# Kernel optimization log

Hardware: AMD Instinct MI355X
Metric: run time of the kernel (lower is better)

Reference implementation:

```python
import jax, jax.numpy as jnp
import numpy as np

EPS = 1e-6
DIM = 384; HEADS = 6; POINTS = 4; LEVELS = 3; HIDDEN = 96
B = 2; H0 = 48; W0 = 48

def layernorm(x, w, b):
    m = jnp.mean(x, -1, keepdims=True)
    v = jnp.var(x, -1, keepdims=True)
    return (x - m) * jax.lax.rsqrt(v + EPS) * w + b

def make_ref_points(shapes):
    # normalized (x, y) pixel centers concatenated over levels -> [N, 2]
    pts = []
    for (Hl, Wl) in shapes:
        ry = (jnp.arange(Hl, dtype=jnp.float32) + 0.5) / Hl
        rx = (jnp.arange(Wl, dtype=jnp.float32) + 0.5) / Wl
        gy, gx = jnp.meshgrid(ry, rx, indexing='ij')
        pts.append(jnp.stack([gx.ravel(), gy.ravel()], -1))
    return jnp.concatenate(pts, 0)

def bilinear_gather(v, x, y, Hl, Wl):
    # v: [B, heads, Hl*Wl, c]; x, y: [B, heads, M] pixel coords
    # matches torch grid_sample(bilinear, align_corners=False, padding zeros)
    x0f = jnp.floor(x); y0f = jnp.floor(y)
    wx = (x - x0f)[..., None]; wy = (y - y0f)[..., None]
    x0 = x0f.astype(jnp.int32); y0 = y0f.astype(jnp.int32)
    def tap(yy, xx):
        valid = ((yy >= 0) & (yy < Hl) & (xx >= 0) & (xx < Wl)).astype(v.dtype)
        idx = jnp.clip(yy, 0, Hl - 1) * Wl + jnp.clip(xx, 0, Wl - 1)
        return jnp.take_along_axis(v, idx[..., None], axis=2) * valid[..., None]
    return (tap(y0, x0) * (1 - wx) * (1 - wy) + tap(y0, x0 + 1) * wx * (1 - wy)
            + tap(y0 + 1, x0) * (1 - wx) * wy + tap(y0 + 1, x0 + 1) * wx * wy)

def msdeform_attn(q, f, shapes, Wv, bv, Woff, boff, Watt, batt, Wout, bout):
    Bq, Nq, C = q.shape
    c = C // HEADS
    value = (f @ Wv + bv).reshape(Bq, -1, HEADS, c)
    off = (q @ Woff + boff).reshape(Bq, Nq, HEADS, LEVELS, POINTS, 2)
    att = jax.nn.softmax((q @ Watt + batt).reshape(Bq, Nq, HEADS, LEVELS * POINTS), -1)
    att = att.reshape(Bq, Nq, HEADS, LEVELS, POINTS)
    ref = make_ref_points(shapes)  # [Nq, 2]
    norm = jnp.array([[wl, hl] for (hl, wl) in shapes], dtype=q.dtype)  # [L, 2] = (W, H)
    loc = ref[None, :, None, None, None, :] + off / norm[None, None, None, :, None, :]
    starts = np.cumsum([0] + [h * w for (h, w) in shapes])
    out = jnp.zeros((Bq, Nq, HEADS, c), q.dtype)
    for l, (Hl, Wl) in enumerate(shapes):
        vl = value[:, starts[l]:starts[l + 1]].transpose(0, 2, 1, 3)  # [B,h,HW,c]
        ll = loc[:, :, :, l]  # [B,N,h,P,2]
        x = (ll[..., 0] * Wl - 0.5).transpose(0, 2, 1, 3).reshape(Bq, HEADS, Nq * POINTS)
        y = (ll[..., 1] * Hl - 0.5).transpose(0, 2, 1, 3).reshape(Bq, HEADS, Nq * POINTS)
        s = bilinear_gather(vl, x, y, Hl, Wl).reshape(Bq, HEADS, Nq, POINTS, c)
        out = out + jnp.einsum('bhnpc,bnhp->bnhc', s, att[:, :, :, l])
    return out.reshape(Bq, Nq, C) @ Wout + bout

def dwconv_levels(x, shapes, dw_w, dw_b):
    Bq, N, C = x.shape
    outs, s = [], 0
    for (Hl, Wl) in shapes:
        xi = x[:, s:s + Hl * Wl].reshape(Bq, Hl, Wl, C)
        yi = jax.lax.conv_general_dilated(xi, dw_w, (1, 1), 'SAME',
             dimension_numbers=('NHWC', 'HWIO', 'NHWC'), feature_group_count=C) + dw_b
        outs.append(yi.reshape(Bq, Hl * Wl, C))
        s += Hl * Wl
    return jnp.concatenate(outs, 1)

def setup_inputs():
    key = jax.random.key(0)
    ks = jax.random.split(key, 16)
    n = (H0 * W0) // 4
    N = 21 * n
    wfn = lambda k, s: 0.02 * jax.random.normal(k, s, jnp.float32)
    ones = lambda s: jnp.ones(s, jnp.float32)
    zeros = lambda s: jnp.zeros(s, jnp.float32)
    return {
        'query': jax.random.normal(ks[0], (B, N, DIM), jnp.float32),
        'reference_points': jax.random.uniform(ks[1], (B, N, 1, 2), dtype=jnp.float32),
        'feat': jax.random.normal(ks[2], (B, 4 * n, DIM), jnp.float32),
        'spatial_shapes': jnp.array([[2 * H0, 2 * W0], [H0, W0], [H0 // 2, W0 // 2]], jnp.int32),
        'level_start_index': jnp.array([0, 16 * n, 20 * n], jnp.int32),
        'H': H0, 'W': W0,
        'cti_qnorm_w': ones((DIM,)), 'cti_qnorm_b': zeros((DIM,)),
        'cti_fnorm_w': ones((DIM,)), 'cti_fnorm_b': zeros((DIM,)),
        'cf_qnorm_w': ones((DIM,)), 'cf_qnorm_b': zeros((DIM,)),
        'cf_fnorm_w': ones((DIM,)), 'cf_fnorm_b': zeros((DIM,)),
        'Wv': wfn(ks[3], (DIM, DIM)), 'bv': zeros((DIM,)),
        'Woff': wfn(ks[4], (DIM, HEADS * LEVELS * POINTS * 2)), 'boff': zeros((HEADS * LEVELS * POINTS * 2,)),
        'Watt': wfn(ks[5], (DIM, HEADS * LEVELS * POINTS)), 'batt': zeros((HEADS * LEVELS * POINTS,)),
        'Wout': wfn(ks[6], (DIM, DIM)), 'bout': zeros((DIM,)),
        'ffn_norm_w': ones((DIM,)), 'ffn_norm_b': zeros((DIM,)),
        'fc1_w': wfn(ks[7], (DIM, HIDDEN)), 'fc1_b': zeros((HIDDEN,)),
        'dw_w': wfn(ks[8], (3, 3, 1, HIDDEN)), 'dw_b': zeros((HIDDEN,)),
        'fc2_w': wfn(ks[9], (HIDDEN, DIM)), 'fc2_b': zeros((DIM,)),
    }

def reference(query, reference_points, feat, spatial_shapes, level_start_index, H, W,
              cti_qnorm_w, cti_qnorm_b, cti_fnorm_w, cti_fnorm_b,
              cf_qnorm_w, cf_qnorm_b, cf_fnorm_w, cf_fnorm_b,
              Wv, bv, Woff, boff, Watt, batt, Wout, bout,
              ffn_norm_w, ffn_norm_b, fc1_w, fc1_b, dw_w, dw_b, fc2_w, fc2_b):
    # NOTE: passed reference_points/spatial_shapes/level_start_index are ignored by
    # CTI_toC.forward; it recomputes them via deform_inputs_only_one(query, 16H, 16W).
    Bq, N, C = query.shape
    n = N // 21
    q = jnp.concatenate([query[:, :16 * n], query[:, 16 * n:20 * n] + feat, query[:, 20 * n:]], 1)
    shapes = [(2 * H, 2 * W), (H, W), (H // 2, W // 2)]
    qn = layernorm(q, cti_qnorm_w, cti_qnorm_b)
    fn = layernorm(q, cti_fnorm_w, cti_fnorm_b)
    aq = layernorm(qn, cf_qnorm_w, cf_qnorm_b)
    af = layernorm(fn, cf_fnorm_w, cf_fnorm_b)
    attn = msdeform_attn(aq, af, shapes, Wv, bv, Woff, boff, Watt, batt, Wout, bout)
    out = qn + attn
    h = layernorm(out, ffn_norm_w, ffn_norm_b) @ fc1_w + fc1_b
    h = dwconv_levels(h, shapes, dw_w, dw_b)
    h = jax.nn.gelu(h, approximate=False)
    h = h @ fc2_w + fc2_b
    return out + h
```

## Files before the change

kernel.cpp:

```cpp
#include <hip/hip_runtime.h>
#include <hip/hip_bf16.h>
#include <hip/hip_fp16.h>
#include <cstdint>
#include <cstddef>

#define NB 2
#define NTOK 12096
#define TOKS (NB * NTOK)
#define DIMC 384
#define NHEADS 6
#define CHD 64

typedef __attribute__((ext_vector_type(8))) __bf16 bf16x8;
typedef __attribute__((ext_vector_type(4))) float f32x4;

__device__ __forceinline__ float wave_reduce_add(float v) {
#pragma unroll
  for (int o = 32; o > 0; o >>= 1) v += __shfl_xor(v, o, 64);
  return v;
}

__device__ __forceinline__ float bf_lo(uint u) {
  union { uint i; float f; } c; c.i = u << 16; return c.f;
}
__device__ __forceinline__ float bf_hi(uint u) {
  union { uint i; float f; } c; c.i = u & 0xffff0000u; return c.f;
}
__device__ __forceinline__ ushort f2bf(float x) {
  union { __hip_bfloat16 b; ushort u; } c; c.b = __float2bfloat16(x); return c.u;
}

__device__ __forceinline__ int xcd_chunk(int bid, int nwg) {
  int xcd = bid & 7, off = bid >> 3;
  int q = nwg >> 3, r = nwg & 7;
  return (xcd < r ? xcd * (q + 1) : r * (q + 1) + (xcd - r) * q) + off;
}

__device__ __forceinline__ void gload16(const ushort* g, ushort* l) {
  __builtin_amdgcn_global_load_lds(
      (const __attribute__((address_space(1))) uint*)g,
      (__attribute__((address_space(3))) uint*)l, 16, 0, 0);
}

__global__ __launch_bounds__(256) void prelude_kernel(
    const float* __restrict__ Wv, const float* __restrict__ Woff,
    const float* __restrict__ Watt, const float* __restrict__ Wo,
    const float* __restrict__ fc1, const float* __restrict__ fc2,
    const float* __restrict__ boff, const float* __restrict__ batt,
    const float* __restrict__ fc1b,
    __hip_bfloat16* __restrict__ Wvt, __hip_bfloat16* __restrict__ Wot,
    __hip_bfloat16* __restrict__ Wofat, __hip_bfloat16* __restrict__ fc1t,
    __hip_bfloat16* __restrict__ fc2t, float* __restrict__ bofat,
    float* __restrict__ fc1bp,
    const float* __restrict__ query, const float* __restrict__ feat,
    const float* __restrict__ w1, const float* __restrict__ b1,
    const float* __restrict__ w2, const float* __restrict__ b2,
    const float* __restrict__ w3, const float* __restrict__ b3,
    const float* __restrict__ w4, const float* __restrict__ b4,
    __hip_bfloat16* __restrict__ qn, __hip_bfloat16* __restrict__ aq,
    __hip_bfloat16* __restrict__ af) {
  if (blockIdx.x < 576) {
    int id = blockIdx.x * 256 + threadIdx.x;
    int k = id % 384, n = id / 384;
    Wvt[(size_t)n * 384 + k] = __float2bfloat16(Wv[(size_t)k * 384 + n]);
    Wot[(size_t)n * 384 + k] = __float2bfloat16(Wo[(size_t)k * 384 + n]);
    if (n < 256) {
      float v = 0.f;
      if (n < 144) v = Woff[(size_t)k * 144 + n];
      else if (n < 216) v = Watt[(size_t)k * 72 + (n - 144)];
      Wofat[(size_t)n * 384 + k] = __float2bfloat16(v);
    }
    if (n < 128)
      fc1t[(size_t)n * 384 + k] = __float2bfloat16(n < 96 ? fc1[(size_t)k * 96 + n] : 0.f);
    if (k < 96)
      fc2t[(size_t)n * 96 + k] = __float2bfloat16(fc2[(size_t)k * 384 + n]);
    if (id < 256) bofat[id] = id < 144 ? boff[id] : (id < 216 ? batt[id - 144] : 0.f);
    if (id < 128) fc1bp[id] = id < 96 ? fc1b[id] : 0.f;
    return;
  }

  int wid = ((blockIdx.x - 576) * blockDim.x + threadIdx.x) >> 6;
  if (wid >= TOKS) return;
  int lane = threadIdx.x & 63;
  int bb = wid / NTOK;
  int nq = wid - bb * NTOK;

  float x[6];
  const float* qp = query + (size_t)wid * DIMC + lane;
#pragma unroll
  for (int i = 0; i < 6; ++i) x[i] = qp[64 * i];
  if (nq >= 9216 && nq < 11520) {
    const float* fp = feat + ((size_t)bb * 2304 + (nq - 9216)) * DIMC + lane;
#pragma unroll
    for (int i = 0; i < 6; ++i) x[i] += fp[64 * i];
  }

  float s = 0.f, ss = 0.f;
#pragma unroll
  for (int i = 0; i < 6; ++i) { s += x[i]; ss += x[i] * x[i]; }
  s = wave_reduce_add(s); ss = wave_reduce_add(ss);
  float mean = s * (1.f / DIMC);
  float rs = rsqrtf(ss * (1.f / DIMC) - mean * mean + 1e-6f);

  float qv[6], fv[6];
  __hip_bfloat16* qnp = qn + (size_t)wid * DIMC + lane;
#pragma unroll
  for (int i = 0; i < 6; ++i) {
    int e = lane + 64 * i;
    float xh = (x[i] - mean) * rs;
    qv[i] = xh * w1[e] + b1[e];
    fv[i] = xh * w2[e] + b2[e];
    qnp[64 * i] = __float2bfloat16(qv[i]);
  }

  s = 0.f; ss = 0.f;
#pragma unroll
  for (int i = 0; i < 6; ++i) { s += qv[i]; ss += qv[i] * qv[i]; }
  s = wave_reduce_add(s); ss = wave_reduce_add(ss);
  float m2 = s * (1.f / DIMC);
  float rs2 = rsqrtf(ss * (1.f / DIMC) - m2 * m2 + 1e-6f);
  __hip_bfloat16* aqp = aq + (size_t)wid * DIMC + lane;
#pragma unroll
  for (int i = 0; i < 6; ++i) {
    int e = lane + 64 * i;
    aqp[64 * i] = __float2bfloat16((qv[i] - m2) * rs2 * w3[e] + b3[e]);
  }

  s = 0.f; ss = 0.f;
#pragma unroll
  for (int i = 0; i < 6; ++i) { s += fv[i]; ss += fv[i] * fv[i]; }
  s = wave_reduce_add(s); ss = wave_reduce_add(ss);
  float m3 = s * (1.f / DIMC);
  float rs3 = rsqrtf(ss * (1.f / DIMC) - m3 * m3 + 1e-6f);
  __hip_bfloat16* afp = af + (size_t)wid * DIMC + lane;
#pragma unroll
  for (int i = 0; i < 6; ++i) {
    int e = lane + 64 * i;
    afp[64 * i] = __float2bfloat16((fv[i] - m3) * rs3 * w4[e] + b4[e]);
  }
}

__global__ __launch_bounds__(256) void ln_kernel(
    const float* __restrict__ x, const float* __restrict__ w,
    const float* __restrict__ b, __hip_bfloat16* __restrict__ y) {
  int wid = (blockIdx.x * blockDim.x + threadIdx.x) >> 6;
  if (wid >= TOKS) return;
  int lane = threadIdx.x & 63;
  float v[6];
  const float* xp = x + (size_t)wid * DIMC + lane;
#pragma unroll
  for (int i = 0; i < 6; ++i) v[i] = xp[64 * i];
  float s = 0.f, ss = 0.f;
#pragma unroll
  for (int i = 0; i < 6; ++i) { s += v[i]; ss += v[i] * v[i]; }
  s = wave_reduce_add(s); ss = wave_reduce_add(ss);
  float mean = s * (1.f / DIMC);
  float rs = rsqrtf(ss * (1.f / DIMC) - mean * mean + 1e-6f);
  __hip_bfloat16* yp = y + (size_t)wid * DIMC + lane;
#pragma unroll
  for (int i = 0; i < 6; ++i) {
    int e = lane + 64 * i;
    yp[64 * i] = __float2bfloat16((v[i] - mean) * rs * w[e] + b[e]);
  }
}

template <int EPI, int OUTBF16>
__global__ __launch_bounds__(256) void gemm_mfma(
    const __hip_bfloat16* __restrict__ A, const __hip_bfloat16* __restrict__ Wt,
    const float* __restrict__ bias, const void* __restrict__ Rv,
    void* __restrict__ Cv, int K, int Np, int ntx) {
  __shared__ __align__(16) ushort As[2 * 128 * 32];
  __shared__ __align__(16) ushort Bs[2 * 128 * 32];
  const int tid = threadIdx.x;
  const int tile = xcd_chunk(blockIdx.x, gridDim.x);
  const int tx = tile % ntx, ty = tile / ntx;
  const int m0 = ty * 128, n0 = tx * 128;

  const int lane = tid & 63, wv = tid >> 6;
  const int wm = (wv >> 1) * 64, wn = (wv & 1) * 64;
  const int rl = lane & 15, kb = lane >> 4;

  const int c0 = wv * 64 + lane;
  const int c1 = c0 + 256;
  const int r0c = c0 >> 2, b0 = (c0 & 3) ^ (r0c & 3);
  const int r1c = c1 >> 2, b1 = (c1 & 3) ^ (r1c & 3);
  const ushort* gA0 = (const ushort*)A + (size_t)(m0 + r0c) * K + b0 * 8;
  const ushort* gA1 = (const ushort*)A + (size_t)(m0 + r1c) * K + b1 * 8;
  const ushort* gB0 = (const ushort*)Wt + (size_t)(n0 + r0c) * K + b0 * 8;
  const ushort* gB1 = (const ushort*)Wt + (size_t)(n0 + r1c) * K + b1 * 8;
  ushort* lA0 = &As[(size_t)wv * 512];
  ushort* lA1 = &As[(size_t)wv * 512 + 2048];
  ushort* lB0 = &Bs[(size_t)wv * 512];
  ushort* lB1 = &Bs[(size_t)wv * 512 + 2048];

  f32x4 acc[4][4] = {};
  const int nt = K >> 5;

  gload16(gA0, lA0);
  gload16(gA1, lA1);
  gload16(gB0, lB0);
  gload16(gB1, lB1);
  __syncthreads();

  for (int t = 0; t < nt; ++t) {
    const int cb = (t & 1) << 12;
    const int nb = 4096 - cb;
    if (t + 1 < nt) {
      const int k1 = (t + 1) << 5;
      gload16(gA0 + k1, lA0 + nb);
      gload16(gA1 + k1, lA1 + nb);
      gload16(gB0 + k1, lB0 + nb);
      gload16(gB1 + k1, lB1 + nb);
    }
    bf16x8 avf[4], bvf[4];
#pragma unroll
    for (int i = 0; i < 4; ++i) {
      int ra = wm + i * 16 + rl;
      avf[i] = *(const bf16x8*)&As[cb + ra * 32 + ((kb ^ (ra & 3)) << 3)];
      int rb = wn + i * 16 + rl;
      bvf[i] = *(const bf16x8*)&Bs[cb + rb * 32 + ((kb ^ (rb & 3)) << 3)];
    }
#pragma unroll
    for (int i = 0; i < 4; ++i)
#pragma unroll
      for (int j = 0; j < 4; ++j)
        acc[i][j] = __builtin_amdgcn_mfma_f32_16x16x32_bf16(avf[i], bvf[j],
                                                            acc[i][j], 0, 0, 0);
    __syncthreads();
  }

#pragma unroll
  for (int i = 0; i < 4; ++i) {
#pragma unroll
    for (int j = 0; j < 4; ++j) {
      int col = n0 + wn + j * 16 + rl;
      float bsv = bias[col];
#pragma unroll
      for (int rr = 0; rr < 4; ++rr) {
        int row = m0 + wm + i * 16 + kb * 4 + rr;
        size_t o = (size_t)row * Np + col;
        float v = acc[i][j][rr] + bsv;
        if (EPI == 1) v += __bfloat162float(((const __hip_bfloat16*)Rv)[o]);
        if (EPI == 2) v += ((const float*)Cv)[o];
        if (OUTBF16) ((__hip_bfloat16*)Cv)[o] = __float2bfloat16(v);
        else ((float*)Cv)[o] = v;
      }
    }
  }
}

__global__ __launch_bounds__(256) void gemm_dual(
    const __hip_bfloat16* __restrict__ A1, const __hip_bfloat16* __restrict__ W1,
    const float* __restrict__ bias1, void* __restrict__ C1,
    const __hip_bfloat16* __restrict__ A2, const __hip_bfloat16* __restrict__ W2,
    const float* __restrict__ bias2, void* __restrict__ C2) {
  __shared__ __align__(16) ushort As[2 * 128 * 32];
  __shared__ __align__(16) ushort Bs[2 * 128 * 32];
  const int tid = threadIdx.x;
  const int gbid = blockIdx.x;
  const bool r2 = gbid >= 567;
  const __hip_bfloat16* A = r2 ? A2 : A1;
  const __hip_bfloat16* Wt = r2 ? W2 : W1;
  const float* bias = r2 ? bias2 : bias1;
  void* Cv = r2 ? C2 : C1;
  const int Np = r2 ? 256 : 384, ntx = r2 ? 2 : 3;
  const int lbid = r2 ? gbid - 567 : gbid;
  const int lnwg = r2 ? 378 : 567;
  const int K = 384;

  const int tile = xcd_chunk(lbid, lnwg);
  const int tx = tile % ntx, ty = tile / ntx;
  const int m0 = ty * 128, n0 = tx * 128;

  const int lane = tid & 63, wv = tid >> 6;
  const int wm = (wv >> 1) * 64, wn = (wv & 1) * 64;
  const int rl = lane & 15, kb = lane >> 4;

  const int c0 = wv * 64 + lane;
  const int c1 = c0 + 256;
  const int r0c = c0 >> 2, b0 = (c0 & 3) ^ (r0c & 3);
  const int r1c = c1 >> 2, b1 = (c1 & 3) ^ (r1c & 3);
  const ushort* gA0 = (const ushort*)A + (size_t)(m0 + r0c) * K + b0 * 8;
  const ushort* gA1 = (const ushort*)A + (size_t)(m0 + r1c) * K + b1 * 8;
  const ushort* gB0 = (const ushort*)Wt + (size_t)(n0 + r0c) * K + b0 * 8;
  const ushort* gB1 = (const ushort*)Wt + (size_t)(n0 + r1c) * K + b1 * 8;
  ushort* lA0 = &As[(size_t)wv * 512];
  ushort* lA1 = &As[(size_t)wv * 512 + 2048];
  ushort* lB0 = &Bs[(size_t)wv * 512];
  ushort* lB1 = &Bs[(size_t)wv * 512 + 2048];

  f32x4 acc[4][4] = {};
  const int nt = K >> 5;

  gload16(gA0, lA0);
  gload16(gA1, lA1);
  gload16(gB0, lB0);
  gload16(gB1, lB1);
  __syncthreads();

  for (int t = 0; t < nt; ++t) {
    const int cb = (t & 1) << 12;
    const int nb = 4096 - cb;
    if (t + 1 < nt) {
      const int k1 = (t + 1) << 5;
      gload16(gA0 + k1, lA0 + nb);
      gload16(gA1 + k1, lA1 + nb);
      gload16(gB0 + k1, lB0 + nb);
      gload16(gB1 + k1, lB1 + nb);
    }
    bf16x8 avf[4], bvf[4];
#pragma unroll
    for (int i = 0; i < 4; ++i) {
      int ra = wm + i * 16 + rl;
      avf[i] = *(const bf16x8*)&As[cb + ra * 32 + ((kb ^ (ra & 3)) << 3)];
      int rb = wn + i * 16 + rl;
      bvf[i] = *(const bf16x8*)&Bs[cb + rb * 32 + ((kb ^ (rb & 3)) << 3)];
    }
#pragma unroll
    for (int i = 0; i < 4; ++i)
#pragma unroll
      for (int j = 0; j < 4; ++j)
        acc[i][j] = __builtin_amdgcn_mfma_f32_16x16x32_bf16(avf[i], bvf[j],
                                                            acc[i][j], 0, 0, 0);
    __syncthreads();
  }

#pragma unroll
  for (int i = 0; i < 4; ++i) {
#pragma unroll
    for (int j = 0; j < 4; ++j) {
      int col = n0 + wn + j * 16 + rl;
      float bsv = bias[col];
#pragma unroll
      for (int rr = 0; rr < 4; ++rr) {
        int row = m0 + wm + i * 16 + kb * 4 + rr;
        size_t o = (size_t)row * Np + col;
        float v = acc[i][j][rr] + bsv;
        if (!r2) ((__hip_bfloat16*)Cv)[o] = __float2bfloat16(v);
        else ((float*)Cv)[o] = v;
      }
    }
  }
}

__global__ __launch_bounds__(256) void msdeform_prep(
    const float* __restrict__ offatt, uint* __restrict__ taps) {
  int tile = xcd_chunk(blockIdx.x, gridDim.x);
  int id = tile * 256 + (int)threadIdx.x;
  if (id >= TOKS * 72) return;
  int t = id / 72, r = id - t * 72;
  int h = r / 12, lp = r - h * 12;
  int l = lp >> 2;
  int nq = t % NTOK;

  int pos, Hq, Wq;
  if (nq < 9216)       { pos = nq;         Hq = 96; Wq = 96; }
  else if (nq < 11520) { pos = nq - 9216;  Hq = 48; Wq = 48; }
  else                 { pos = nq - 11520; Hq = 24; Wq = 24; }
  int iq = pos / Wq, jq = pos - iq * Wq;
  float refx = (jq + 0.5f) / (float)Wq;
  float refy = (iq + 0.5f) / (float)Hq;

  const float* lg = offatt + (size_t)t * 256 + 144 + h * 12;
  float mx = -1e30f;
#pragma unroll
  for (int i = 0; i < 12; ++i) mx = fmaxf(mx, lg[i]);
  float sden = 0.f;
#pragma unroll
  for (int i = 0; i < 12; ++i) sden += __expf(lg[i] - mx);
  float aw = __expf(lg[lp] - mx) / sden;

  float ox = offatt[(size_t)t * 256 + h * 24 + lp * 2 + 0];
  float oy = offatt[(size_t)t * 256 + h * 24 + lp * 2 + 1];

  int Wl = 96 >> l;

  float xx = refx * (float)Wl + ox - 0.5f;
  float yy = refy * (float)Wl + oy - 0.5f;
  float x0f = floorf(xx), y0f = floorf(yy);
  int x0 = (int)x0f, y0 = (int)y0f;
  float wx = xx - x0f, wy = yy - y0f;

  bool vx0 = (x0 >= 0) & (x0 < Wl), vx1 = (x0 + 1 >= 0) & (x0 + 1 < Wl);
  bool vy0 = (y0 >= 0) & (y0 < Wl), vy1 = (y0 + 1 >= 0) & (y0 + 1 < Wl);
  int x0c = min(max(x0, 0), Wl - 1), x1c = min(max(x0 + 1, 0), Wl - 1);
  int y0c = min(max(y0, 0), Wl - 1), y1c = min(max(y0 + 1, 0), Wl - 1);

  float w00 = (vy0 && vx0) ? aw * (1.f - wx) * (1.f - wy) : 0.f;
  float w01 = (vy0 && vx1) ? aw * wx * (1.f - wy) : 0.f;
  float w10 = (vy1 && vx0) ? aw * (1.f - wx) * wy : 0.f;
  float w11 = (vy1 && vx1) ? aw * wx * wy : 0.f;

  uint4 rec;
  rec.x = ((uint)f2bf(w00) << 16) | (uint)(y0c * Wl + x0c);
  rec.y = ((uint)f2bf(w01) << 16) | (uint)(y0c * Wl + x1c);
  rec.z = ((uint)f2bf(w10) << 16) | (uint)(y1c * Wl + x0c);
  rec.w = ((uint)f2bf(w11) << 16) | (uint)(y1c * Wl + x1c);
  *(uint4*)&taps[((size_t)(t * NHEADS + h)) * 48 + lp * 4] = rec;
}

__global__ __launch_bounds__(256) void msdeform_gather(
    const __hip_bfloat16* __restrict__ value, const uint* __restrict__ taps,
    __hip_bfloat16* __restrict__ samp) {
  int swz = xcd_chunk(blockIdx.x, gridDim.x);
  int wid = __builtin_amdgcn_readfirstlane(swz * 4 + ((int)threadIdx.x >> 6));
  int lane = threadIdx.x & 63;
  int g = lane >> 3, sub = lane & 7;
  int sub16 = sub * 16;

  int t = wid / NHEADS;
  int h = wid - t * NHEADS;
  int b = t / NTOK;

  const char* vb = (const char*)value + ((size_t)(b * NTOK) * DIMC + h * CHD) * 2;
  const char* vbl[3] = {vb, vb + 9216 * DIMC * 2, vb + 11520 * DIMC * 2};

  const uint* tp = taps + (size_t)wid * 48 + g;

  float acc[8] = {0.f, 0.f, 0.f, 0.f, 0.f, 0.f, 0.f, 0.f};
#pragma unroll
  for (int i = 0; i < 6; ++i) {
    uint rec = tp[i * 8];
    float wf = bf_hi(rec);
    uint off = (rec & 0x3fffu) * (uint)(DIMC * 2) + (uint)sub16;
    uint4 d = *(const uint4*)(vbl[i >> 1] + off);
    acc[0] = fmaf(wf, bf_lo(d.x), acc[0]);
    acc[1] = fmaf(wf, bf_hi(d.x), acc[1]);
    acc[2] = fmaf(wf, bf_lo(d.y), acc[2]);
    acc[3] = fmaf(wf, bf_hi(d.y), acc[3]);
    acc[4] = fmaf(wf, bf_lo(d.z), acc[4]);
    acc[5] = fmaf(wf, bf_hi(d.z), acc[5]);
    acc[6] = fmaf(wf, bf_lo(d.w), acc[6]);
    acc[7] = fmaf(wf, bf_hi(d.w), acc[7]);
  }

#pragma unroll
  for (int r = 0; r < 8; ++r) {
    acc[r] += __shfl_xor(acc[r], 8, 64);
    acc[r] += __shfl_xor(acc[r], 16, 64);
    acc[r] += __shfl_xor(acc[r], 32, 64);
  }

  if (lane < 8) {
    uint4 o;
    o.x = ((uint)f2bf(acc[1]) << 16) | f2bf(acc[0]);
    o.y = ((uint)f2bf(acc[3]) << 16) | f2bf(acc[2]);
    o.z = ((uint)f2bf(acc[5]) << 16) | f2bf(acc[4]);
    o.w = ((uint)f2bf(acc[7]) << 16) | f2bf(acc[6]);
    *(uint4*)((char*)samp + (size_t)wid * 128 + sub16) = o;
  }
}

__global__ __launch_bounds__(256) void dwconv_gelu(
    const __hip_bfloat16* __restrict__ x, const float* __restrict__ w,
    const float* __restrict__ bias, __hip_bfloat16* __restrict__ y) {
  int id = blockIdx.x * blockDim.x + threadIdx.x;
  if (id >= TOKS * 24) return;
  int g = id % 24;
  int tn = id / 24;
  int ch0 = g * 4;
  int b = tn / NTOK, nq = tn - b * NTOK;

  int pos, Hl, Wl, st;
  if (nq < 9216)       { pos = nq;         Hl = 96; Wl = 96; st = 0; }
  else if (nq < 11520) { pos = nq - 9216;  Hl = 48; Wl = 48; st = 9216; }
  else                 { pos = nq - 11520; Hl = 24; Wl = 24; st = 11520; }
  int i = pos / Wl, j = pos - i * Wl;

  f32x4 acc = *(const f32x4*)&bias[ch0];
#pragma unroll
  for (int di = 0; di < 3; ++di) {
#pragma unroll
    for (int dj = 0; dj < 3; ++dj) {
      int ii = i + di - 1, jj = j + dj - 1;
      if (ii >= 0 && ii < Hl && jj >= 0 && jj < Wl) {
        uint2 d = *(const uint2*)&x[((size_t)(b * NTOK + st + ii * Wl + jj)) * 128 + ch0];
        f32x4 wv = *(const f32x4*)&w[(di * 3 + dj) * 96 + ch0];
        acc[0] = fmaf(bf_lo(d.x), wv[0], acc[0]);
        acc[1] = fmaf(bf_hi(d.x), wv[1], acc[1]);
        acc[2] = fmaf(bf_lo(d.y), wv[2], acc[2]);
        acc[3] = fmaf(bf_hi(d.y), wv[3], acc[3]);
      }
    }
  }
  uint2 o;
  float g0 = 0.5f * acc[0] * (1.f + erff(acc[0] * 0.70710678f));
  float g1 = 0.5f * acc[1] * (1.f + erff(acc[1] * 0.70710678f));
  float g2 = 0.5f * acc[2] * (1.f + erff(acc[2] * 0.70710678f));
  float g3 = 0.5f * acc[3] * (1.f + erff(acc[3] * 0.70710678f));
  o.x = ((uint)f2bf(g1) << 16) | f2bf(g0);
  o.y = ((uint)f2bf(g3) << 16) | f2bf(g2);
  *(uint2*)((char*)y + (size_t)tn * 192 + ch0 * 2) = o;
}

extern "C" void kernel_launch(void* const* d_in, const int* in_sizes, int n_in,
                              void* d_out, int out_size, void* d_ws, size_t ws_size,
                              hipStream_t stream) {
  const float* query = (const float*)d_in[0];
  const float* feat   = (const float*)d_in[2];
  const float* cti_qw = (const float*)d_in[7];
  const float* cti_qb = (const float*)d_in[8];
  const float* cti_fw = (const float*)d_in[9];
  const float* cti_fb = (const float*)d_in[10];
  const float* cf_qw  = (const float*)d_in[11];
  const float* cf_qb  = (const float*)d_in[12];
  const float* cf_fw  = (const float*)d_in[13];
  const float* cf_fb  = (const float*)d_in[14];
  const float* Wv     = (const float*)d_in[15];
  const float* bv     = (const float*)d_in[16];
  const float* Woff   = (const float*)d_in[17];
  const float* boff   = (const float*)d_in[18];
  const float* Watt   = (const float*)d_in[19];
  const float* batt   = (const float*)d_in[20];
  const float* Wo     = (const float*)d_in[21];
  const float* bo     = (const float*)d_in[22];
  const float* ffw    = (const float*)d_in[23];
  const float* ffb    = (const float*)d_in[24];
  const float* fc1w   = (const float*)d_in[25];
  const float* fc1b   = (const float*)d_in[26];
  const float* dww    = (const float*)d_in[27];
  const float* dwb    = (const float*)d_in[28];
  const float* fc2w   = (const float*)d_in[29];
  const float* fc2b   = (const float*)d_in[30];
  float* out = (float*)d_out;

  char* ws = (char*)d_ws;
  __hip_bfloat16* qn  = (__hip_bfloat16*)ws;
  __hip_bfloat16* aq  = (__hip_bfloat16*)(ws + 37158912);
  __hip_bfloat16* af  = (__hip_bfloat16*)(ws + 55738368);
  __hip_bfloat16* val = (__hip_bfloat16*)(ws + 74317824);
  float* offatt       = (float*)(ws + 92897280);
  char* wbase = ws + 117669888;
  __hip_bfloat16* Wvt   = (__hip_bfloat16*)(wbase + 0);
  __hip_bfloat16* Wot   = (__hip_bfloat16*)(wbase + 589824);
  __hip_bfloat16* Wofat = (__hip_bfloat16*)(wbase + 1179648);
  __hip_bfloat16* fc1t  = (__hip_bfloat16*)(wbase + 1376256);
  __hip_bfloat16* fc2t  = (__hip_bfloat16*)(wbase + 1474560);
  float* bofat          = (float*)(wbase + 1548288);
  float* fc1bp          = (float*)(wbase + 1549312);
  uint* taps = (uint*)(ws + 119220224);
  __hip_bfloat16* samp = af;
  __hip_bfloat16* lnf  = aq;
  __hip_bfloat16* h1   = (__hip_bfloat16*)offatt;
  __hip_bfloat16* h2   = (__hip_bfloat16*)(ws + 92897280 + 6193152);

  dim3 blk(256);

  prelude_kernel<<<576 + TOKS / 4, blk, 0, stream>>>(
      Wv, Woff, Watt, Wo, fc1w, fc2w, boff, batt, fc1b, Wvt, Wot, Wofat, fc1t,
      fc2t, bofat, fc1bp, query, feat, cti_qw, cti_qb, cti_fw, cti_fb, cf_qw,
      cf_qb, cf_fw, cf_fb, qn, aq, af);

  gemm_dual<<<945, blk, 0, stream>>>(af, Wvt, bv, val, aq, Wofat, bofat, offatt);

  msdeform_prep<<<(TOKS * 72) / 256, blk, 0, stream>>>(offatt, taps);
  msdeform_gather<<<(TOKS * NHEADS) / 4, blk, 0, stream>>>(val, taps, samp);

  gemm_mfma<1, 0><<<567, blk, 0, stream>>>(samp, Wot, bo, qn, out, 384, 384, 3);

  ln_kernel<<<TOKS / 4, blk, 0, stream>>>(out, ffw, ffb, lnf);
  gemm_mfma<0, 1><<<189, blk, 0, stream>>>(lnf, fc1t, fc1bp, nullptr, h1, 384, 128, 1);
  dwconv_gelu<<<(TOKS * 24 + 255) / 256, blk, 0, stream>>>(h1, dww, dwb, h2);
  gemm_mfma<2, 0><<<567, blk, 0, stream>>>(h2, fc2t, fc2b, nullptr, out, 96, 384, 3);
}
```

Measured before the change: 185.6 us.

## Fold FFN layernorm into out-proj epilogue stats and fc1 GEMM epilogue

Removes the standalone layernorm kernel. The Wout GEMM epilogue now writes a bf16 copy of its output and accumulates per-row sum and sum-of-squares with atomics. The fc1 GEMM runs on the raw output, with the LN weight folded into fc1 and the mean/rstd correction applied algebraically in its epilogue. This saves one full read and write pass over the activations, but adds atomics and a stats buffer zeroed inside the gather kernel. Feeding raw activations to bf16 changes numerics slightly.

```diff
diff --git a/kernel.cpp b/kernel.cpp
--- a/kernel.cpp
+++ b/kernel.cpp
@@ -47,11 +47,12 @@
     const float* __restrict__ Watt, const float* __restrict__ Wo,
     const float* __restrict__ fc1, const float* __restrict__ fc2,
     const float* __restrict__ boff, const float* __restrict__ batt,
-    const float* __restrict__ fc1b,
+    const float* __restrict__ fc1b, const float* __restrict__ ffw,
+    const float* __restrict__ ffb,
     __hip_bfloat16* __restrict__ Wvt, __hip_bfloat16* __restrict__ Wot,
     __hip_bfloat16* __restrict__ Wofat, __hip_bfloat16* __restrict__ fc1t,
     __hip_bfloat16* __restrict__ fc2t, float* __restrict__ bofat,
-    float* __restrict__ fc1bp,
+    float* __restrict__ fcs, float* __restrict__ fcc,
     const float* __restrict__ query, const float* __restrict__ feat,
     const float* __restrict__ w1, const float* __restrict__ b1,
     const float* __restrict__ w2, const float* __restrict__ b2,
@@ -71,11 +72,25 @@
       Wofat[(size_t)n * 384 + k] = __float2bfloat16(v);
     }
     if (n < 128)
-      fc1t[(size_t)n * 384 + k] = __float2bfloat16(n < 96 ? fc1[(size_t)k * 96 + n] : 0.f);
+      fc1t[(size_t)n * 384 + k] =
+          __float2bfloat16(n < 96 ? ffw[k] * fc1[(size_t)k * 96 + n] : 0.f);
     if (k < 96)
       fc2t[(size_t)n * 96 + k] = __float2bfloat16(fc2[(size_t)k * 384 + n]);
     if (id < 256) bofat[id] = id < 144 ? boff[id] : (id < 216 ? batt[id - 144] : 0.f);
-    if (id < 128) fc1bp[id] = id < 96 ? fc1b[id] : 0.f;
+    if (blockIdx.x == 0 && threadIdx.x < 128) {
+      int n = threadIdx.x;
+      float s = 0.f, c = 0.f;
+      if (n < 96) {
+        for (int kk = 0; kk < 384; ++kk) {
+          float w = fc1[(size_t)kk * 96 + n];
+          s += ffw[kk] * w;
+          c += ffb[kk] * w;
+        }
+        c += fc1b[n];
+      }
+      fcs[n] = s;
+      fcc[n] = c;
+    }
     return;
   }
 
@@ -137,30 +152,6 @@
   for (int i = 0; i < 6; ++i) {
     int e = lane + 64 * i;
     afp[64 * i] = __float2bfloat16((fv[i] - m3) * rs3 * w4[e] + b4[e]);
-  }
-}
-
-__global__ __launch_bounds__(256) void ln_kernel(
-    const float* __restrict__ x, const float* __restrict__ w,
-    const float* __restrict__ b, __hip_bfloat16* __restrict__ y) {
-  int wid = (blockIdx.x * blockDim.x + threadIdx.x) >> 6;
-  if (wid >= TOKS) return;
-  int lane = threadIdx.x & 63;
-  float v[6];
-  const float* xp = x + (size_t)wid * DIMC + lane;
-#pragma unroll
-  for (int i = 0; i < 6; ++i) v[i] = xp[64 * i];
-  float s = 0.f, ss = 0.f;
-#pragma unroll
-  for (int i = 0; i < 6; ++i) { s += v[i]; ss += v[i] * v[i]; }
-  s = wave_reduce_add(s); ss = wave_reduce_add(ss);
-  float mean = s * (1.f / DIMC);
-  float rs = rsqrtf(ss * (1.f / DIMC) - mean * mean + 1e-6f);
-  __hip_bfloat16* yp = y + (size_t)wid * DIMC + lane;
-#pragma unroll
-  for (int i = 0; i < 6; ++i) {
-    int e = lane + 64 * i;
-    yp[64 * i] = __float2bfloat16((v[i] - mean) * rs * w[e] + b[e]);
   }
 }
 
@@ -244,6 +235,193 @@
         if (EPI == 2) v += ((const float*)Cv)[o];
         if (OUTBF16) ((__hip_bfloat16*)Cv)[o] = __float2bfloat16(v);
         else ((float*)Cv)[o] = v;
+      }
+    }
+  }
+}
+
+__global__ __launch_bounds__(256) void gemm_wout(
+    const __hip_bfloat16* __restrict__ A, const __hip_bfloat16* __restrict__ Wt,
+    const float* __restrict__ bias, const __hip_bfloat16* __restrict__ Rv,
+    float* __restrict__ out, __hip_bfloat16* __restrict__ outbf,
+    float* __restrict__ stats) {
+  __shared__ __align__(16) ushort As[2 * 128 * 32];
+  __shared__ __align__(16) ushort Bs[2 * 128 * 32];
+  const int K = 384, Np = 384, ntx = 3;
+  const int tid = threadIdx.x;
+  const int tile = xcd_chunk(blockIdx.x, gridDim.x);
+  const int tx = tile % ntx, ty = tile / ntx;
+  const int m0 = ty * 128, n0 = tx * 128;
+
+  const int lane = tid & 63, wv = tid >> 6;
+  const int wm = (wv >> 1) * 64, wn = (wv & 1) * 64;
+  const int rl = lane & 15, kb = lane >> 4;
+
+  const int c0 = wv * 64 + lane;
+  const int c1 = c0 + 256;
+  const int r0c = c0 >> 2, b0 = (c0 & 3) ^ (r0c & 3);
+  const int r1c = c1 >> 2, b1 = (c1 & 3) ^ (r1c & 3);
+  const ushort* gA0 = (const ushort*)A + (size_t)(m0 + r0c) * K + b0 * 8;
+  const ushort* gA1 = (const ushort*)A + (size_t)(m0 + r1c) * K + b1 * 8;
+  const ushort* gB0 = (const ushort*)Wt + (size_t)(n0 + r0c) * K + b0 * 8;
+  const ushort* gB1 = (const ushort*)Wt + (size_t)(n0 + r1c) * K + b1 * 8;
+  ushort* lA0 = &As[(size_t)wv * 512];
+  ushort* lA1 = &As[(size_t)wv * 512 + 2048];
+  ushort* lB0 = &Bs[(size_t)wv * 512];
+  ushort* lB1 = &Bs[(size_t)wv * 512 + 2048];
+
+  f32x4 acc[4][4] = {};
+  const int nt = K >> 5;
+
+  gload16(gA0, lA0);
+  gload16(gA1, lA1);
+  gload16(gB0, lB0);
+  gload16(gB1, lB1);
+  __syncthreads();
+
+  for (int t = 0; t < nt; ++t) {
+    const int cb = (t & 1) << 12;
+    const int nb = 4096 - cb;
+    if (t + 1 < nt) {
+      const int k1 = (t + 1) << 5;
+      gload16(gA0 + k1, lA0 + nb);
+      gload16(gA1 + k1, lA1 + nb);
+      gload16(gB0 + k1, lB0 + nb);
+      gload16(gB1 + k1, lB1 + nb);
+    }
+    bf16x8 avf[4], bvf[4];
+#pragma unroll
+    for (int i = 0; i < 4; ++i) {
+      int ra = wm + i * 16 + rl;
+      avf[i] = *(const bf16x8*)&As[cb + ra * 32 + ((kb ^ (ra & 3)) << 3)];
+      int rb = wn + i * 16 + rl;
+      bvf[i] = *(const bf16x8*)&Bs[cb + rb * 32 + ((kb ^ (rb & 3)) << 3)];
+    }
+#pragma unroll
+    for (int i = 0; i < 4; ++i)
+#pragma unroll
+      for (int j = 0; j < 4; ++j)
+        acc[i][j] = __builtin_amdgcn_mfma_f32_16x16x32_bf16(avf[i], bvf[j],
+                                                            acc[i][j], 0, 0, 0);
+    __syncthreads();
+  }
+
+  float s1a[4][4] = {}, s2a[4][4] = {};
+#pragma unroll
+  for (int i = 0; i < 4; ++i) {
+#pragma unroll
+    for (int j = 0; j < 4; ++j) {
+      int col = n0 + wn + j * 16 + rl;
+      float bsv = bias[col];
+#pragma unroll
+      for (int rr = 0; rr < 4; ++rr) {
+        int row = m0 + wm + i * 16 + kb * 4 + rr;
+        size_t o = (size_t)row * Np + col;
+        float v = acc[i][j][rr] + bsv +
+                  __bfloat162float(Rv[o]);
+        out[o] = v;
+        outbf[o] = __float2bfloat16(v);
+        s1a[i][rr] += v;
+        s2a[i][rr] += v * v;
+      }
+    }
+  }
+#pragma unroll
+  for (int i = 0; i < 4; ++i) {
+#pragma unroll
+    for (int rr = 0; rr < 4; ++rr) {
+      float a = s1a[i][rr], bq = s2a[i][rr];
+      a += __shfl_xor(a, 1, 64);  bq += __shfl_xor(bq, 1, 64);
+      a += __shfl_xor(a, 2, 64);  bq += __shfl_xor(bq, 2, 64);
+      a += __shfl_xor(a, 4, 64);  bq += __shfl_xor(bq, 4, 64);
+      a += __shfl_xor(a, 8, 64);  bq += __shfl_xor(bq, 8, 64);
+      if (rl == 0) {
+        int row = m0 + wm + i * 16 + kb * 4 + rr;
+        atomicAdd(&stats[row * 2 + 0], a);
+        atomicAdd(&stats[row * 2 + 1], bq);
+      }
+    }
+  }
+}
+
+__global__ __launch_bounds__(256) void gemm_fc1(
+    const __hip_bfloat16* __restrict__ A, const __hip_bfloat16* __restrict__ Wt,
+    const float* __restrict__ stats, const float* __restrict__ fcs,
+    const float* __restrict__ fcc, __hip_bfloat16* __restrict__ C) {
+  __shared__ __align__(16) ushort As[2 * 128 * 32];
+  __shared__ __align__(16) ushort Bs[2 * 128 * 32];
+  const int K = 384, Np = 128;
+  const int tid = threadIdx.x;
+  const int tile = xcd_chunk(blockIdx.x, gridDim.x);
+  const int m0 = tile * 128, n0 = 0;
+
+  const int lane = tid & 63, wv = tid >> 6;
+  const int wm = (wv >> 1) * 64, wn = (wv & 1) * 64;
+  const int rl = lane & 15, kb = lane >> 4;
+
+  const int c0 = wv * 64 + lane;
+  const int c1 = c0 + 256;
+  const int r0c = c0 >> 2, b0 = (c0 & 3) ^ (r0c & 3);
+  const int r1c = c1 >> 2, b1 = (c1 & 3) ^ (r1c & 3);
+  const ushort* gA0 = (const ushort*)A + (size_t)(m0 + r0c) * K + b0 * 8;
+  const ushort* gA1 = (const ushort*)A + (size_t)(m0 + r1c) * K + b1 * 8;
+  const ushort* gB0 = (const ushort*)Wt + (size_t)(n0 + r0c) * K + b0 * 8;
+  const ushort* gB1 = (const ushort*)Wt + (size_t)(n0 + r1c) * K + b1 * 8;
+  ushort* lA0 = &As[(size_t)wv * 512];
+  ushort* lA1 = &As[(size_t)wv * 512 + 2048];
+  ushort* lB0 = &Bs[(size_t)wv * 512];
+  ushort* lB1 = &Bs[(size_t)wv * 512 + 2048];
+
+  f32x4 acc[4][4] = {};
+  const int nt = K >> 5;
+
+  gload16(gA0, lA0);
+  gload16(gA1, lA1);
+  gload16(gB0, lB0);
+  gload16(gB1, lB1);
+  __syncthreads();
+
+  for (int t = 0; t < nt; ++t) {
+    const int cb = (t & 1) << 12;
+    const int nb = 4096 - cb;
+    if (t + 1 < nt) {
+      const int k1 = (t + 1) << 5;
+      gload16(gA0 + k1, lA0 + nb);
+      gload16(gA1 + k1, lA1 + nb);
+      gload16(gB0 + k1, lB0 + nb);
+      gload16(gB1 + k1, lB1 + nb);
+    }
+    bf16x8 avf[4], bvf[4];
+#pragma unroll
+    for (int i = 0; i < 4; ++i) {
+      int ra = wm + i * 16 + rl;
+      avf[i] = *(const bf16x8*)&As[cb + ra * 32 + ((kb ^ (ra & 3)) << 3)];
+      int rb = wn + i * 16 + rl;
+      bvf[i] = *(const bf16x8*)&Bs[cb + rb * 32 + ((kb ^ (rb & 3)) << 3)];
+    }
+#pragma unroll
+    for (int i = 0; i < 4; ++i)
+#pragma unroll
+      for (int j = 0; j < 4; ++j)
+        acc[i][j] = __builtin_amdgcn_mfma_f32_16x16x32_bf16(avf[i], bvf[j],
+                                                            acc[i][j], 0, 0, 0);
+    __syncthreads();
+  }
+
+#pragma unroll
+  for (int i = 0; i < 4; ++i) {
+#pragma unroll
+    for (int rr = 0; rr < 4; ++rr) {
+      int row = m0 + wm + i * 16 + kb * 4 + rr;
+      float sm = stats[row * 2 + 0];
+      float sq = stats[row * 2 + 1];
+      float mu = sm * (1.f / 384.f);
+      float rs = rsqrtf(sq * (1.f / 384.f) - mu * mu + 1e-6f);
+#pragma unroll
+      for (int j = 0; j < 4; ++j) {
+        int col = wn + j * 16 + rl;
+        float v = rs * (acc[i][j][rr] - mu * fcs[col]) + fcc[col];
+        C[(size_t)row * Np + col] = __float2bfloat16(v);
       }
     }
   }
@@ -401,7 +579,9 @@
 
 __global__ __launch_bounds__(256) void msdeform_gather(
     const __hip_bfloat16* __restrict__ value, const uint* __restrict__ taps,
-    __hip_bfloat16* __restrict__ samp) {
+    __hip_bfloat16* __restrict__ samp, float* __restrict__ stats) {
+  if (blockIdx.x < 189) stats[blockIdx.x * 256 + threadIdx.x] = 0.f;
+
   int swz = xcd_chunk(blockIdx.x, gridDim.x);
   int wid = __builtin_amdgcn_readfirstlane(swz * 4 + ((int)threadIdx.x >> 6));
   int lane = threadIdx.x & 63;
@@ -537,29 +717,31 @@
   __hip_bfloat16* fc1t  = (__hip_bfloat16*)(wbase + 1376256);
   __hip_bfloat16* fc2t  = (__hip_bfloat16*)(wbase + 1474560);
   float* bofat          = (float*)(wbase + 1548288);
-  float* fc1bp          = (float*)(wbase + 1549312);
+  float* fcs            = (float*)(wbase + 1549312);
+  float* fcc            = (float*)(wbase + 1549824);
   uint* taps = (uint*)(ws + 119220224);
-  __hip_bfloat16* samp = af;
-  __hip_bfloat16* lnf  = aq;
-  __hip_bfloat16* h1   = (__hip_bfloat16*)offatt;
-  __hip_bfloat16* h2   = (__hip_bfloat16*)(ws + 92897280 + 6193152);
+  __hip_bfloat16* samp  = af;
+  __hip_bfloat16* outbf = val;
+  __hip_bfloat16* h1    = (__hip_bfloat16*)offatt;
+  __hip_bfloat16* h2    = (__hip_bfloat16*)(ws + 92897280 + 6193152);
+  float* stats          = (float*)(ws + 92897280 + 6193152 + 4644864);
 
   dim3 blk(256);
 
   prelude_kernel<<<576 + TOKS / 4, blk, 0, stream>>>(
-      Wv, Woff, Watt, Wo, fc1w, fc2w, boff, batt, fc1b, Wvt, Wot, Wofat, fc1t,
-      fc2t, bofat, fc1bp, query, feat, cti_qw, cti_qb, cti_fw, cti_fb, cf_qw,
-      cf_qb, cf_fw, cf_fb, qn, aq, af);
+      Wv, Woff, Watt, Wo, fc1w, fc2w, boff, batt, fc1b, ffw, ffb, Wvt, Wot,
+      Wofat, fc1t, fc2t, bofat, fcs, fcc, query, feat, cti_qw, cti_qb, cti_fw,
+      cti_fb, cf_qw, cf_qb, cf_fw, cf_fb, qn, aq, af);
 
   gemm_dual<<<945, blk, 0, stream>>>(af, Wvt, bv, val, aq, Wofat, bofat, offatt);
 
   msdeform_prep<<<(TOKS * 72) / 256, blk, 0, stream>>>(offatt, taps);
-  msdeform_gather<<<(TOKS * NHEADS) / 4, blk, 0, stream>>>(val, taps, samp);
-
-  gemm_mfma<1, 0><<<567, blk, 0, stream>>>(samp, Wot, bo, qn, out, 384, 384, 3);
-
-  ln_kernel<<<TOKS / 4, blk, 0, stream>>>(out, ffw, ffb, lnf);
-  gemm_mfma<0, 1><<<189, blk, 0, stream>>>(lnf, fc1t, fc1bp, nullptr, h1, 384, 128, 1);
+  msdeform_gather<<<(TOKS * NHEADS) / 4, blk, 0, stream>>>(val, taps, samp, stats);
+
+  gemm_wout<<<567, blk, 0, stream>>>(samp, Wot, bo, qn, out, outbf, stats);
+
+  gemm_fc1<<<189, blk, 0, stream>>>(outbf, fc1t, stats, fcs, fcc, h1);
+
   dwconv_gelu<<<(TOKS * 24 + 255) / 256, blk, 0, stream>>>(h1, dww, dwb, h2);
   gemm_mfma<2, 0><<<567, blk, 0, stream>>>(h2, fc2t, fc2b, nullptr, out, 96, 384, 3);
 }
```

After: 197.7 us. 6.5% more time.
